# Kernel tuning notes

Measured on AMD Instinct MI355X. Metric: run time of the kernel, lower is better.

## Reference

```python
import jax, jax.numpy as jnp
import numpy as np

N, E, F, H, C, K = 50000, 1600000, 128, 64, 40, 4


def setup_inputs() -> dict:
    key = jax.random.key(0)
    ks = jax.random.split(key, 4)
    x = jax.random.normal(ks[0], (N, F), dtype=jnp.float32)
    edge_index = jax.random.randint(ks[1], (2, E), 0, N, dtype=jnp.int32)
    edge_weight = jnp.ones((E,), dtype=jnp.float32)
    # lin of ChebConv: Linear(K*in, out); kaiming for layer1, xavier-ish for layer2
    W1 = jax.random.normal(ks[2], (K * F, H), dtype=jnp.float32) * (2.0 / (K * F)) ** 0.5
    b1 = jnp.zeros((H,), jnp.float32)
    W2 = jax.random.normal(ks[3], (K * H, C), dtype=jnp.float32) * (2.0 / (K * H + C)) ** 0.5
    b2 = jnp.zeros((C,), jnp.float32)
    return {"x": x, "edge_index": edge_index, "edge_weight": edge_weight,
            "W1": W1, "b1": b1, "W2": W2, "b2": b2}


def _cheb_norm(edge_index, edge_weight, num_nodes):
    """Edge weights of L_hat = 2*L/lambda_max - I with sym norm, lambda_max=2.
    L = I - D^{-1/2} A D^{-1/2}; so L_hat off-diag = -d_i^{-1/2} w d_j^{-1/2},
    diag = (1 if deg>0 else 0) - 1."""
    src, dst = edge_index[0], edge_index[1]
    deg = jax.ops.segment_sum(edge_weight, src, num_segments=num_nodes)
    dis = jnp.where(deg > 0, jax.lax.rsqrt(jnp.maximum(deg, 1e-12)), 0.0)
    w_norm = -dis[src] * edge_weight * dis[dst]   # [E] off-diagonal of L_hat
    diag = jnp.where(deg > 0, 0.0, -1.0)          # [N] diagonal of L_hat
    return src, dst, w_norm, diag


def _cheb_conv(x, src, dst, w_norm, diag, W, b, num_nodes):
    def prop(h):  # L_hat @ h via gather-multiply-scatter
        msg = w_norm[:, None] * h[src]                                  # [E, F]
        return diag[:, None] * h + jax.ops.segment_sum(msg, dst, num_segments=num_nodes)

    Tx_prev2 = x
    Tx_prev1 = prop(x)
    Txs = [Tx_prev2, Tx_prev1]
    for _ in range(2, K):
        Tx = 2.0 * prop(Tx_prev1) - Tx_prev2
        Txs.append(Tx)
        Tx_prev2, Tx_prev1 = Tx_prev1, Tx
    Z = jnp.concatenate(Txs, axis=1)              # [N, K*F]
    return Z @ W + b


def reference(x, edge_index, edge_weight, W1, b1, W2, b2):
    num_nodes = x.shape[0]
    src, dst, w_norm, diag = _cheb_norm(edge_index, edge_weight, num_nodes)
    # dropout layers are identity at inference
    h = _cheb_conv(x, src, dst, w_norm, diag, W1, b1, num_nodes)
    h = jax.nn.relu(h)
    out = _cheb_conv(h, src, dst, w_norm, diag, W2, b2, num_nodes)
    return out
```

## Files before the change

kernel.cpp:

```cpp
#include <hip/hip_runtime.h>

#define NN 50000
#define EE 1600000
#define FF 128
#define HH 64
#define CC 40

#define NCH 64
#define CHE (EE / NCH)
#define NSL 4
#define SLN (NN / NSL)

#define PA 250
#define EPP (EE / PA)
#define SB 250
#define SLNB 200
#define BCAP 64

static __device__ __forceinline__ float bf2f(unsigned short u) {
    union { unsigned int i; float f; } c; c.i = ((unsigned int)u) << 16; return c.f;
}
static __device__ __forceinline__ unsigned short f2bf(float x) {
    union { float f; unsigned int i; } c; c.f = x;
    unsigned int r = c.i + 0x7FFFu + ((c.i >> 16) & 1u);
    return (unsigned short)(r >> 16);
}

__global__ __launch_bounds__(1024) void deg_hist_kernel(
    const int* __restrict__ src, const float* __restrict__ w,
    float* __restrict__ pdeg) {
    __shared__ float ldeg[SLN];
    int s = blockIdx.x % NSL;
    int c = blockIdx.x / NSL;
    int base = s * SLN;
    for (int i = threadIdx.x; i < SLN; i += 1024) ldeg[i] = 0.f;
    __syncthreads();
    int e0 = c * CHE;
    for (int e = e0 + threadIdx.x; e < e0 + CHE; e += 1024) {
        int se = src[e];
        unsigned us = (unsigned)(se - base);
        if (us < SLN) atomicAdd(&ldeg[us], w[e]);
    }
    __syncthreads();
    for (int i = threadIdx.x; i < SLN; i += 1024)
        pdeg[(size_t)c * NN + base + i] = ldeg[i];
}

__global__ void reduce_kernel(const float* __restrict__ pdeg,
                              float* __restrict__ dis, float* __restrict__ diag) {
    int n = blockIdx.x * blockDim.x + threadIdx.x;
    if (n >= NN) return;
    float dsum = 0.f;
    for (int c = 0; c < NCH; ++c) dsum += pdeg[(size_t)c * NN + n];
    dis[n]  = (dsum > 0.f) ? rsqrtf(fmaxf(dsum, 1e-12f)) : 0.f;
    diag[n] = (dsum > 0.f) ? 0.f : -1.f;
}

__global__ __launch_bounds__(256) void bucketA_kernel(
    const int* __restrict__ src, const int* __restrict__ dst,
    const float* __restrict__ w, const float* __restrict__ dis,
    uint2* __restrict__ buckets, int* __restrict__ counts) {
    __shared__ int lcnt[SB];
    int p = blockIdx.x;
    for (int i = threadIdx.x; i < SB; i += 256) lcnt[i] = 0;
    __syncthreads();
    int e0 = p * EPP;
    for (int e = e0 + threadIdx.x; e < e0 + EPP; e += 256) {
        int de = dst[e], se = src[e];
        int sl = de / SLNB;
        int dl = de - sl * SLNB;
        float wn = -dis[se] * w[e] * dis[de];
        unsigned lo = (unsigned)se | ((unsigned)f2bf(wn) << 16);
        int idx = atomicAdd(&lcnt[sl], 1);
        buckets[((size_t)p * SB + sl) * BCAP + idx] = make_uint2(lo, (unsigned)dl);
    }
    __syncthreads();
    for (int i = threadIdx.x; i < SB; i += 256) counts[p * SB + i] = lcnt[i];
}

__global__ void scanS_kernel(const int* __restrict__ counts, int* __restrict__ sbase) {
    __shared__ int sh[256];
    int t = threadIdx.x;
    int total = 0;
    if (t < SB)
        for (int p = 0; p < PA; ++p) total += counts[p * SB + t];
    sh[t] = total;
    __syncthreads();
    for (int off = 1; off < 256; off <<= 1) {
        int x = (t >= off) ? sh[t - off] : 0;
        __syncthreads();
        sh[t] += x;
        __syncthreads();
    }
    if (t < SB) sbase[t] = sh[t] - total;
    if (t == SB - 1) sbase[SB] = sh[t];
}

__global__ __launch_bounds__(256) void bucketB_kernel(
    const uint2* __restrict__ buckets, const int* __restrict__ counts,
    const int* __restrict__ sbase,
    int* __restrict__ row_start, unsigned int* __restrict__ csr) {
    __shared__ int lcounts[PA];
    __shared__ int lhist[SLNB];
    __shared__ int sh[256];
    int s = blockIdx.x;
    int t = threadIdx.x;
    if (t < PA) lcounts[t] = counts[t * SB + s];
    for (int i = t; i < SLNB; i += 256) lhist[i] = 0;
    __syncthreads();
    int g = t >> 4, l16 = t & 15;
    for (int p = g; p < PA; p += 16) {
        int c = lcounts[p];
        const uint2* b = buckets + ((size_t)p * SB + s) * BCAP;
        for (int i = l16; i < c; i += 16)
            atomicAdd(&lhist[b[i].y], 1);
    }
    __syncthreads();
    int v = (t < SLNB) ? lhist[t] : 0;
    sh[t] = v;
    __syncthreads();
    for (int off = 1; off < 256; off <<= 1) {
        int x = (t >= off) ? sh[t - off] : 0;
        __syncthreads();
        sh[t] += x;
        __syncthreads();
    }
    int base = sbase[s];
    if (t < SLNB) {
        int excl = sh[t] - v;
        row_start[s * SLNB + t] = base + excl;
        lhist[t] = base + excl;
    }
    if (s == SB - 1 && t == 0) row_start[NN] = sbase[SB];
    __syncthreads();
    for (int p = g; p < PA; p += 16) {
        int c = lcounts[p];
        const uint2* b = buckets + ((size_t)p * SB + s) * BCAP;
        for (int i = l16; i < c; i += 16) {
            uint2 en = b[i];
            int pos = atomicAdd(&lhist[en.y], 1);
            csr[pos] = en.x;
        }
    }
}

template <int FACT, typename OUT_T>
__global__ __launch_bounds__(256) void prop2_kernel(
    const unsigned short* __restrict__ a, float alphaL,
    const unsigned short* __restrict__ p1, float beta1,
    const unsigned short* __restrict__ p2, float beta2,
    const float* __restrict__ bias, int doRelu, int FOUT, int outStride,
    const float* __restrict__ diag, const int* __restrict__ rs,
    const unsigned int* __restrict__ csr, OUT_T* __restrict__ out) {
    int lane = threadIdx.x & 63;
    int wave = threadIdx.x >> 6;
    int n = blockIdx.x * 4 + wave;
    int f = lane;
    float acc = 0.f;
    if (f < FACT) {
        acc = diag[n] * bf2f(a[(size_t)n * 64 + f]);
        int j0 = rs[n], j1 = rs[n + 1];
        int j = j0;
        for (; j + 8 <= j1; j += 8) {
            unsigned cw[8];
            #pragma unroll
            for (int u = 0; u < 8; ++u) cw[u] = csr[j + u];
            float v[8];
            #pragma unroll
            for (int u = 0; u < 8; ++u)
                v[u] = bf2f(a[(size_t)(cw[u] & 0xFFFFu) * 64 + f]);
            #pragma unroll
            for (int u = 0; u < 8; ++u)
                acc = fmaf(bf2f((unsigned short)(cw[u] >> 16)), v[u], acc);
        }
        for (; j < j1; ++j) {
            unsigned cw = csr[j];
            acc = fmaf(bf2f((unsigned short)(cw >> 16)),
                       bf2f(a[(size_t)(cw & 0xFFFFu) * 64 + f]), acc);
        }
    }
    if (f < FOUT) {
        float r = alphaL * acc + beta1 * bf2f(p1[(size_t)n * 64 + f]);
        if (beta2 != 0.f) r = fmaf(beta2, bf2f(p2[(size_t)n * 64 + f]), r);
        if (bias) r += bias[f];
        if (doRelu) r = fmaxf(r, 0.f);
        OUT_T o;
        if constexpr (sizeof(OUT_T) == 2) o = f2bf(r); else o = r;
        out[(size_t)n * outStride + f] = o;
    }
}

__global__ __launch_bounds__(256) void gemm1_kernel(
    const float* __restrict__ x, const float* __restrict__ W,
    unsigned short* __restrict__ Yb) {
    __shared__ float As[64][36];
    __shared__ float Bs[32][64];
    int t = threadIdx.x;
    int m0 = blockIdx.x * 64;
    int ct = blockIdx.y;
    int tr = t / 16, tc = t % 16;
    int kq = t % 8,  ms = t / 8;
    int jb = t % 16, fb = t / 16;
    float acc[4][4] = {};
    for (int kb = 0; kb < 4; ++kb) {
        __syncthreads();
        #pragma unroll
        for (int p = 0; p < 2; ++p) {
            int m = ms + 32 * p;
            int row = m0 + m;
            float4 vv = make_float4(0.f, 0.f, 0.f, 0.f);
            if (row < NN) vv = *(const float4*)(x + (size_t)row * FF + kb * 32 + kq * 4);
            *(float4*)&As[m][kq * 4] = vv;
        }
        const float* Wb = W + ((size_t)ct * 128 + kb * 32) * HH;
        #pragma unroll
        for (int p = 0; p < 2; ++p) {
            int fi = fb + 16 * p;
            float4 vv = *(const float4*)(Wb + fi * HH + jb * 4);
            *(float4*)&Bs[fi][jb * 4] = vv;
        }
        __syncthreads();
        #pragma unroll 8
        for (int k = 0; k < 32; ++k) {
            float a0 = As[tr * 4 + 0][k], a1 = As[tr * 4 + 1][k];
            float a2 = As[tr * 4 + 2][k], a3 = As[tr * 4 + 3][k];
            float4 b = *(float4*)&Bs[k][tc * 4];
            acc[0][0] = fmaf(a0, b.x, acc[0][0]); acc[0][1] = fmaf(a0, b.y, acc[0][1]);
            acc[0][2] = fmaf(a0, b.z, acc[0][2]); acc[0][3] = fmaf(a0, b.w, acc[0][3]);
            acc[1][0] = fmaf(a1, b.x, acc[1][0]); acc[1][1] = fmaf(a1, b.y, acc[1][1]);
            acc[1][2] = fmaf(a1, b.z, acc[1][2]); acc[1][3] = fmaf(a1, b.w, acc[1][3]);
            acc[2][0] = fmaf(a2, b.x, acc[2][0]); acc[2][1] = fmaf(a2, b.y, acc[2][1]);
            acc[2][2] = fmaf(a2, b.z, acc[2][2]); acc[2][3] = fmaf(a2, b.w, acc[2][3]);
            acc[3][0] = fmaf(a3, b.x, acc[3][0]); acc[3][1] = fmaf(a3, b.y, acc[3][1]);
            acc[3][2] = fmaf(a3, b.z, acc[3][2]); acc[3][3] = fmaf(a3, b.w, acc[3][3]);
        }
    }
    unsigned short* slab = Yb + (size_t)ct * NN * 64;
    #pragma unroll
    for (int r = 0; r < 4; ++r) {
        int n = m0 + tr * 4 + r;
        if (n < NN) {
            ushort4 u4;
            u4.x = f2bf(acc[r][0]); u4.y = f2bf(acc[r][1]);
            u4.z = f2bf(acc[r][2]); u4.w = f2bf(acc[r][3]);
            *(ushort4*)(slab + (size_t)n * 64 + tc * 4) = u4;
        }
    }
}

__global__ __launch_bounds__(256) void gemm2_kernel(
    const float* __restrict__ h, const float* __restrict__ W,
    unsigned short* __restrict__ Zb) {
    __shared__ float As[128][36];
    __shared__ float Bs[32][40];
    int t = threadIdx.x;
    int m0 = blockIdx.x * 128;
    int kt = blockIdx.y;
    int tr = t / 8, tc = t % 8;
    int kq = t % 8, ms = t / 8;
    float acc[4][5] = {};
    for (int kb = 0; kb < 2; ++kb) {
        __syncthreads();
        #pragma unroll
        for (int p = 0; p < 4; ++p) {
            int m = ms + 32 * p;
            int row = m0 + m;
            float4 vv = make_float4(0.f, 0.f, 0.f, 0.f);
            if (row < NN) vv = *(const float4*)(h + (size_t)row * HH + kb * 32 + kq * 4);
            *(float4*)&As[m][kq * 4] = vv;
        }
        const float* Wb = W + ((size_t)kt * 64 + kb * 32) * CC;
        for (int i = t; i < 32 * CC; i += 256) ((float*)Bs)[i] = Wb[i];
        __syncthreads();
        #pragma unroll 4
        for (int k = 0; k < 32; ++k) {
            float a0 = As[tr * 4 + 0][k], a1 = As[tr * 4 + 1][k];
            float a2 = As[tr * 4 + 2][k], a3 = As[tr * 4 + 3][k];
            #pragma unroll
            for (int c = 0; c < 5; ++c) {
                float b = Bs[k][tc * 5 + c];
                acc[0][c] = fmaf(a0, b, acc[0][c]);
                acc[1][c] = fmaf(a1, b, acc[1][c]);
                acc[2][c] = fmaf(a2, b, acc[2][c]);
                acc[3][c] = fmaf(a3, b, acc[3][c]);
            }
        }
    }
    unsigned short* slab = Zb + (size_t)kt * NN * 64;
    #pragma unroll
    for (int r = 0; r < 4; ++r) {
        int n = m0 + tr * 4 + r;
        if (n < NN) {
            unsigned short* brow = slab + (size_t)n * 64;
            #pragma unroll
            for (int c = 0; c < 5; ++c) brow[tc * 5 + c] = f2bf(acc[r][c]);
            if (tc < 6) {
                #pragma unroll
                for (int c = 0; c < 4; ++c) brow[40 + tc * 4 + c] = 0;
            }
        }
    }
}

extern "C" void kernel_launch(void* const* d_in, const int* in_sizes, int n_in,
                              void* d_out, int out_size, void* d_ws, size_t ws_size,
                              hipStream_t stream) {
    const float* x    = (const float*)d_in[0];
    const int*   eidx = (const int*)d_in[1];
    const float* ew   = (const float*)d_in[2];
    const float* W1   = (const float*)d_in[3];
    const float* b1   = (const float*)d_in[4];
    const float* W2   = (const float*)d_in[5];
    const float* b2   = (const float*)d_in[6];
    float* out = (float*)d_out;

    const int* src = eidx;
    const int* dst = eidx + EE;

    float* p = (float*)d_ws;
    unsigned int* csr = (unsigned int*)p;  p += (size_t)EE;
    float* dis  = p;                  p += ((NN + 63) / 64) * 64;
    float* diag = p;                  p += ((NN + 63) / 64) * 64;
    unsigned short* Yb = (unsigned short*)p;  p += (size_t)NN * 128;
    unsigned short* u  = (unsigned short*)p;  p += (size_t)NN * 32;
    unsigned short* v  = (unsigned short*)p;  p += (size_t)NN * 32;
    float* h    = p;                  p += (size_t)NN * 64;
    float* scratch = p;               p += (size_t)PA * SB * BCAP * 2;
    int* row_start = (int*)p;
    int* counts    = row_start + NN + 1;
    int* sbase     = counts + PA * SB;

    float* pdeg    = scratch;
    uint2* buckets = (uint2*)scratch;
    unsigned short* y0b = Yb;
    unsigned short* y1b = Yb + (size_t)1 * NN * 64;
    unsigned short* y2b = Yb + (size_t)2 * NN * 64;
    unsigned short* y3b = Yb + (size_t)3 * NN * 64;
    unsigned short* Zb = Yb;
    unsigned short* z0 = Zb;
    unsigned short* z1 = Zb + (size_t)1 * NN * 64;
    unsigned short* z2 = Zb + (size_t)2 * NN * 64;
    unsigned short* z3 = Zb + (size_t)3 * NN * 64;
    unsigned short* u2 = u;
    unsigned short* v2 = v;

    const int B = 256;
    deg_hist_kernel<<<NCH * NSL, 1024, 0, stream>>>(src, ew, pdeg);
    reduce_kernel<<<(NN + B - 1) / B, B, 0, stream>>>(pdeg, dis, diag);
    bucketA_kernel<<<PA, 256, 0, stream>>>(src, dst, ew, dis, buckets, counts);
    scanS_kernel<<<1, 256, 0, stream>>>(counts, sbase);
    bucketB_kernel<<<SB, 256, 0, stream>>>(buckets, counts, sbase, row_start, csr);

    int pgrid = NN / 4;

    gemm1_kernel<<<dim3((NN + 63) / 64, 4), 256, 0, stream>>>(x, W1, Yb);
    prop2_kernel<64, unsigned short><<<pgrid, 256, 0, stream>>>(
        y3b, 4.f, y2b, 2.f, nullptr, 0.f,
        nullptr, 0, 64, 64, diag, row_start, csr, u);
    prop2_kernel<64, unsigned short><<<pgrid, 256, 0, stream>>>(
        u, 1.f, y1b, 1.f, y3b, -3.f,
        nullptr, 0, 64, 64, diag, row_start, csr, v);
    prop2_kernel<64, float><<<pgrid, 256, 0, stream>>>(
        v, 1.f, y0b, 1.f, y2b, -1.f,
        b1, 1, 64, 64, diag, row_start, csr, h);

    gemm2_kernel<<<dim3((NN + 127) / 128, 4), 256, 0, stream>>>(h, W2, Zb);
    prop2_kernel<48, unsigned short><<<pgrid, 256, 0, stream>>>(
        z3, 4.f, z2, 2.f, nullptr, 0.f,
        nullptr, 0, 48, 64, diag, row_start, csr, u2);
    prop2_kernel<48, unsigned short><<<pgrid, 256, 0, stream>>>(
        u2, 1.f, z1, 1.f, z3, -3.f,
        nullptr, 0, 48, 64, diag, row_start, csr, v2);
    prop2_kernel<48, float><<<pgrid, 256, 0, stream>>>(
        v2, 1.f, z0, 1.f, z2, -1.f,
        b2, 0, 40, 40, diag, row_start, csr, out);
}
```

Baseline: 525.5 us.

## Load x tile once per block and loop over all four weight slabs in gemm1

The first GEMM now stages the full 64x128 x tile in shared memory once per block and loops over the four Chebyshev weight slabs inside the block, instead of launching a separate grid column per slab that re-reads x each time. The inner loop also reads A as float4 vectors rather than scalars. This cuts global traffic on x by a factor of four and the number of shared-memory load instructions, at the cost of more shared memory per block (about 42 KB) and fewer, longer-running blocks.

```diff
diff --git a/kernel.cpp b/kernel.cpp
--- a/kernel.cpp
+++ b/kernel.cpp
@@ -193,57 +193,67 @@
 __global__ __launch_bounds__(256) void gemm1_kernel(
     const float* __restrict__ x, const float* __restrict__ W,
     unsigned short* __restrict__ Yb) {
-    __shared__ float As[64][36];
+    __shared__ float As[64][132];
     __shared__ float Bs[32][64];
     int t = threadIdx.x;
     int m0 = blockIdx.x * 64;
-    int ct = blockIdx.y;
+    #pragma unroll
+    for (int p = 0; p < 8; ++p) {
+        int idx = p * 256 + t;
+        int row = idx >> 5;
+        int f4  = idx & 31;
+        int grow = m0 + row;
+        float4 vv = make_float4(0.f, 0.f, 0.f, 0.f);
+        if (grow < NN) vv = *(const float4*)(x + (size_t)grow * FF + f4 * 4);
+        *(float4*)&As[row][f4 * 4] = vv;
+    }
     int tr = t / 16, tc = t % 16;
-    int kq = t % 8,  ms = t / 8;
     int jb = t % 16, fb = t / 16;
-    float acc[4][4] = {};
-    for (int kb = 0; kb < 4; ++kb) {
-        __syncthreads();
+    for (int ct = 0; ct < 4; ++ct) {
+        float acc[4][4] = {};
+        for (int kb = 0; kb < 4; ++kb) {
+            __syncthreads();
+            const float* Wb = W + ((size_t)ct * 128 + kb * 32) * HH;
+            #pragma unroll
+            for (int p = 0; p < 2; ++p) {
+                int fi = fb + 16 * p;
+                float4 vv = *(const float4*)(Wb + fi * HH + jb * 4);
+                *(float4*)&Bs[fi][jb * 4] = vv;
+            }
+            __syncthreads();
+            #pragma unroll
+            for (int k4 = 0; k4 < 8; ++k4) {
+                int k0 = kb * 32 + k4 * 4;
+                float4 a0 = *(float4*)&As[tr * 4 + 0][k0];
+                float4 a1 = *(float4*)&As[tr * 4 + 1][k0];
+                float4 a2 = *(float4*)&As[tr * 4 + 2][k0];
+                float4 a3 = *(float4*)&As[tr * 4 + 3][k0];
+                #pragma unroll
+                for (int i = 0; i < 4; ++i) {
+                    float4 b = *(float4*)&Bs[k4 * 4 + i][tc * 4];
+                    float e0 = (&a0.x)[i], e1 = (&a1.x)[i];
+                    float e2 = (&a2.x)[i], e3 = (&a3.x)[i];
+                    acc[0][0] = fmaf(e0, b.x, acc[0][0]); acc[0][1] = fmaf(e0, b.y, acc[0][1]);
+                    acc[0][2] = fmaf(e0, b.z, acc[0][2]); acc[0][3] = fmaf(e0, b.w, acc[0][3]);
+                    acc[1][0] = fmaf(e1, b.x, acc[1][0]); acc[1][1] = fmaf(e1, b.y, acc[1][1]);
+                    acc[1][2] = fmaf(e1, b.z, acc[1][2]); acc[1][3] = fmaf(e1, b.w, acc[1][3]);
+                    acc[2][0] = fmaf(e2, b.x, acc[2][0]); acc[2][1] = fmaf(e2, b.y, acc[2][1]);
+                    acc[2][2] = fmaf(e2, b.z, acc[2][2]); acc[2][3] = fmaf(e2, b.w, acc[2][3]);
+                    acc[3][0] = fmaf(e3, b.x, acc[3][0]); acc[3][1] = fmaf(e3, b.y, acc[3][1]);
+                    acc[3][2] = fmaf(e3, b.z, acc[3][2]); acc[3][3] = fmaf(e3, b.w, acc[3][3]);
+                }
+            }
+        }
+        unsigned short* slab = Yb + (size_t)ct * NN * 64;
         #pragma unroll
-        for (int p = 0; p < 2; ++p) {
-            int m = ms + 32 * p;
-            int row = m0 + m;
-            float4 vv = make_float4(0.f, 0.f, 0.f, 0.f);
-            if (row < NN) vv = *(const float4*)(x + (size_t)row * FF + kb * 32 + kq * 4);
-            *(float4*)&As[m][kq * 4] = vv;
-        }
-        const float* Wb = W + ((size_t)ct * 128 + kb * 32) * HH;
-        #pragma unroll
-        for (int p = 0; p < 2; ++p) {
-            int fi = fb + 16 * p;
-            float4 vv = *(const float4*)(Wb + fi * HH + jb * 4);
-            *(float4*)&Bs[fi][jb * 4] = vv;
-        }
-        __syncthreads();
-        #pragma unroll 8
-        for (int k = 0; k < 32; ++k) {
-            float a0 = As[tr * 4 + 0][k], a1 = As[tr * 4 + 1][k];
-            float a2 = As[tr * 4 + 2][k], a3 = As[tr * 4 + 3][k];
-            float4 b = *(float4*)&Bs[k][tc * 4];
-            acc[0][0] = fmaf(a0, b.x, acc[0][0]); acc[0][1] = fmaf(a0, b.y, acc[0][1]);
-            acc[0][2] = fmaf(a0, b.z, acc[0][2]); acc[0][3] = fmaf(a0, b.w, acc[0][3]);
-            acc[1][0] = fmaf(a1, b.x, acc[1][0]); acc[1][1] = fmaf(a1, b.y, acc[1][1]);
-            acc[1][2] = fmaf(a1, b.z, acc[1][2]); acc[1][3] = fmaf(a1, b.w, acc[1][3]);
-            acc[2][0] = fmaf(a2, b.x, acc[2][0]); acc[2][1] = fmaf(a2, b.y, acc[2][1]);
-            acc[2][2] = fmaf(a2, b.z, acc[2][2]); acc[2][3] = fmaf(a2, b.w, acc[2][3]);
-            acc[3][0] = fmaf(a3, b.x, acc[3][0]); acc[3][1] = fmaf(a3, b.y, acc[3][1]);
-            acc[3][2] = fmaf(a3, b.z, acc[3][2]); acc[3][3] = fmaf(a3, b.w, acc[3][3]);
-        }
-    }
-    unsigned short* slab = Yb + (size_t)ct * NN * 64;
-    #pragma unroll
-    for (int r = 0; r < 4; ++r) {
-        int n = m0 + tr * 4 + r;
-        if (n < NN) {
-            ushort4 u4;
-            u4.x = f2bf(acc[r][0]); u4.y = f2bf(acc[r][1]);
-            u4.z = f2bf(acc[r][2]); u4.w = f2bf(acc[r][3]);
-            *(ushort4*)(slab + (size_t)n * 64 + tc * 4) = u4;
+        for (int r = 0; r < 4; ++r) {
+            int n = m0 + tr * 4 + r;
+            if (n < NN) {
+                ushort4 u4;
+                u4.x = f2bf(acc[r][0]); u4.y = f2bf(acc[r][1]);
+                u4.z = f2bf(acc[r][2]); u4.w = f2bf(acc[r][3]);
+                *(ushort4*)(slab + (size_t)n * 64 + tc * 4) = u4;
+            }
         }
     }
 }
@@ -353,7 +363,7 @@
 
     int pgrid = NN / 4;
 
-    gemm1_kernel<<<dim3((NN + 63) / 64, 4), 256, 0, stream>>>(x, W1, Yb);
+    gemm1_kernel<<<(NN + 63) / 64, 256, 0, stream>>>(x, W1, Yb);
     prop2_kernel<64, unsigned short><<<pgrid, 256, 0, stream>>>(
         y3b, 4.f, y2b, 2.f, nullptr, 0.f,
         nullptr, 0, 64, 64, diag, row_start, csr, u);
```

Measured after the change: 548.1 us. +4.3%, slower.
